# Kernel tuning notes

Measured on AMD Instinct MI355X. Metric: run time of the kernel, lower is better.

The kernel has to match this reference:

```python
import jax, jax.numpy as jnp
import numpy as np

B, L, H, F, D = 8, 2048, 1024, 256, 3  # batch, seq, d_model, adapter bottleneck, non-news domains
EPS = 1e-6  # annotated-transformer LayerNorm eps


def setup_inputs() -> dict:
    key = jax.random.key(0)
    ks = jax.random.split(key, 6)
    s1 = 1.0 / np.sqrt(H)
    s2 = 1.0 / np.sqrt(F)
    return {
        "x": jax.random.normal(ks[0], (B, L, H), jnp.float32),
        # per-domain LayerNorm params (SublayerConnection.norm)
        "ln_g": jnp.ones((D, H), jnp.float32),
        "ln_b": jnp.zeros((D, H), jnp.float32),
        # per-domain adapter FFN: Linear(H->F), ReLU, Linear(F->H)
        "W1": (jax.random.normal(ks[1], (D, F, H), jnp.float32) * s1),
        "b1": jnp.zeros((D, F), jnp.float32),
        "W2": (jax.random.normal(ks[2], (D, H, F), jnp.float32) * s2),
        "b2": jnp.zeros((D, H), jnp.float32),
        # per-domain gate Linear(2H -> 1), split into the x-half (gu) and adapter-half (gv)
        "gu": (jax.random.normal(ks[3], (D, H), jnp.float32) * s1),
        "gv": (jax.random.normal(ks[4], (D, H), jnp.float32) * s1),
        "gb": jnp.zeros((D,), jnp.float32),
    }


def reference(x, ln_g, ln_b, W1, b1, W2, b2, gu, gv, gb):
    # mix_output=True, used_domain_list=['news','book','bible','iwslt'],
    # target_domain='book' (in list -> no extra pass), dropout=eval (identity).
    mu = jnp.mean(x, axis=-1, keepdims=True)
    sd = jnp.std(x, axis=-1, keepdims=True, ddof=1)  # torch .std default (unbiased)
    xn = (x - mu) / (sd + EPS)                        # shared normalization stats
    # per-domain LayerNorm affine -> [D,B,L,H]
    h = xn[None] * ln_g[:, None, None, :] + ln_b[:, None, None, :]
    # adapter FFN (wo_residual_forward): Linear -> ReLU -> Linear
    mid = jax.nn.relu(jnp.einsum('dblh,dfh->dblf', h, W1) + b1[:, None, None, :])
    a = jnp.einsum('dblf,dhf->dblh', mid, W2) + b2[:, None, None, :]  # [D,B,L,H]
    # gate = sigmoid(Linear([x; a])) with W_gate split as [gu | gv]
    gate = jax.nn.sigmoid(
        jnp.einsum('blh,dh->dbl', x, gu)
        + jnp.einsum('dblh,dh->dbl', a, gv)
        + gb[:, None, None]
    )  # [D,B,L]
    # stacked sum includes 'news' contribution (= x), then outer residual +x:
    return 2.0 * x + jnp.sum(gate[..., None] * a, axis=0)
```

## Files before the change

### kernel.cpp

```cpp
#include <hip/hip_runtime.h>
#include <cstdint>

#define T_TOK 16384
#define H 1024
#define F 256
#define D 3
#define DF 768

typedef unsigned short u16;
typedef __attribute__((ext_vector_type(8))) short short8;
typedef __attribute__((ext_vector_type(4))) float floatx4;

__device__ __forceinline__ u16 f2bf(float f) {
  unsigned u = __float_as_uint(f);
  u += 0x7fff + ((u >> 16) & 1);
  return (u16)(u >> 16);
}
__device__ __forceinline__ float bf2f(u16 s) {
  return __uint_as_float(((unsigned)s) << 16);
}

__device__ __forceinline__ void gload_lds16(const void* g, void* l) {
  __builtin_amdgcn_global_load_lds(
      reinterpret_cast<const __attribute__((address_space(1))) void*>(
          reinterpret_cast<uintptr_t>(g)),
      reinterpret_cast<__attribute__((address_space(3))) void*>(
          reinterpret_cast<uintptr_t>(l)),
      16, 0, 0);
}

#define FENCE() asm volatile("" ::: "memory")
#define BAR1() do { FENCE(); __builtin_amdgcn_s_barrier(); \
    asm volatile("s_waitcnt lgkmcnt(0)" ::: "memory"); \
    __builtin_amdgcn_sched_barrier(0); } while (0)
#define BAR2() do { FENCE(); __builtin_amdgcn_s_barrier(); FENCE(); } while (0)
#define VMC(n) asm volatile("s_waitcnt vmcnt(" #n ")" ::: "memory")

__device__ __forceinline__ float block_reduce_256(float v, float* red, int tid) {
  #pragma unroll
  for (int o = 32; o > 0; o >>= 1) v += __shfl_xor(v, o);
  __syncthreads();
  if ((tid & 63) == 0) red[tid >> 6] = v;
  __syncthreads();
  return red[0] + red[1] + red[2] + red[3];
}


__global__ __launch_bounds__(256)
void prep_elem(const float* __restrict__ W1, const float* __restrict__ lng,
               u16* __restrict__ W1p, const float* __restrict__ W2,
               u16* __restrict__ W2r)
{
  int idx = blockIdx.x * 256 + threadIdx.x;
  int stride = gridDim.x * 256;
  for (int i = idx; i < D * F * H; i += stride) {
    int h = i & (H - 1);
    int d = i / (F * H);
    W1p[i] = f2bf(W1[i] * lng[d * H + h]);
  }
  for (int i = idx; i < H * DF; i += stride) {
    int k = i % DF;
    int hh = i / DF;
    int d = k >> 8;
    int f = k & (F - 1);
    W2r[i] = f2bf(W2[((size_t)d * H + hh) * F + f]);
  }
}

__global__ __launch_bounds__(256)
void prep_dots(const float* __restrict__ W1, const float* __restrict__ lnb,
               const float* __restrict__ b1, const float* __restrict__ W2,
               const float* __restrict__ gv, const float* __restrict__ b2,
               const float* __restrict__ gb, float* __restrict__ b1p,
               float* __restrict__ wg, float* __restrict__ cg)
{
  __shared__ float red[4];
  int d = blockIdx.x >> 8;
  int f = blockIdx.x & 255;
  int tid = threadIdx.x;
  float s1 = 0.f, s2 = 0.f, s3 = 0.f;
  for (int h = tid; h < H; h += 256) {
    float w1v = W1[((size_t)d * F + f) * H + h];
    float gvv = gv[d * H + h];
    s1 += lnb[d * H + h] * w1v;
    s2 += W2[((size_t)d * H + h) * F + f] * gvv;
    if (f == 0) s3 += b2[d * H + h] * gvv;
  }
  float S1 = block_reduce_256(s1, red, tid);
  float S2 = block_reduce_256(s2, red, tid);
  if (tid == 0) {
    b1p[d * F + f] = b1[d * F + f] + S1;
    wg[d * F + f] = S2;
  }
  if (f == 0) {
    float S3 = block_reduce_256(s3, red, tid);
    if (tid == 0) cg[d] = gb[d] + S3;
  }
}

__global__ __launch_bounds__(256)
void ln_xu_kernel(const float* __restrict__ x, const float* __restrict__ gu,
                  u16* __restrict__ xn, float* __restrict__ xu)
{
  int t = blockIdx.x;
  int tid = threadIdx.x;
  const float4 xv = *reinterpret_cast<const float4*>(x + (size_t)t * H + tid * 4);
  const float4 g0 = *reinterpret_cast<const float4*>(gu + tid * 4);
  const float4 g1 = *reinterpret_cast<const float4*>(gu + H + tid * 4);
  const float4 g2 = *reinterpret_cast<const float4*>(gu + 2 * H + tid * 4);
  float s  = xv.x + xv.y + xv.z + xv.w;
  float sq = xv.x * xv.x + xv.y * xv.y + xv.z * xv.z + xv.w * xv.w;
  float d0 = xv.x * g0.x + xv.y * g0.y + xv.z * g0.z + xv.w * g0.w;
  float d1 = xv.x * g1.x + xv.y * g1.y + xv.z * g1.z + xv.w * g1.w;
  float d2 = xv.x * g2.x + xv.y * g2.y + xv.z * g2.z + xv.w * g2.w;
  #pragma unroll
  for (int o = 32; o > 0; o >>= 1) {
    s  += __shfl_xor(s, o);  sq += __shfl_xor(sq, o);
    d0 += __shfl_xor(d0, o); d1 += __shfl_xor(d1, o); d2 += __shfl_xor(d2, o);
  }
  __shared__ float red[4][5];
  int w = tid >> 6;
  if ((tid & 63) == 0) {
    red[w][0] = s; red[w][1] = sq; red[w][2] = d0; red[w][3] = d1; red[w][4] = d2;
  }
  __syncthreads();
  float S  = red[0][0] + red[1][0] + red[2][0] + red[3][0];
  float SQ = red[0][1] + red[1][1] + red[2][1] + red[3][1];
  float mu = S * (1.0f / H);
  float var = (SQ - (float)H * mu * mu) * (1.0f / (H - 1));
  float rs = 1.0f / (sqrtf(fmaxf(var, 0.0f)) + 1e-6f);
  ushort4 o4;
  o4.x = f2bf((xv.x - mu) * rs);
  o4.y = f2bf((xv.y - mu) * rs);
  o4.z = f2bf((xv.z - mu) * rs);
  o4.w = f2bf((xv.w - mu) * rs);
  *reinterpret_cast<ushort4*>(xn + (size_t)t * H + tid * 4) = o4;
  if (tid == 0) {
    xu[t]             = red[0][2] + red[1][2] + red[2][2] + red[3][2];
    xu[T_TOK + t]     = red[0][3] + red[1][3] + red[2][3] + red[3][3];
    xu[2 * T_TOK + t] = red[0][4] + red[1][4] + red[2][4] + red[3][4];
  }
}

template <int K, int NLD, int EPI>
__global__ __launch_bounds__(512, 2)
void gemm8(const u16* __restrict__ A, const u16* __restrict__ Bm,
           const float* __restrict__ p0,
           const float* __restrict__ p1,
           const float* __restrict__ p2,
           const float* __restrict__ p3,
           u16* __restrict__ o16,
           float* __restrict__ o32,
           int nBy)
{
  constexpr int NKT = K / 64;
  constexpr int NITER = NKT / 2;
  extern __shared__ u16 LD[];

  const int tid = threadIdx.x, lane = tid & 63, w = tid >> 6;
  const int wm = w >> 2, wn = w & 3, lr = lane & 15, sl = lane >> 4;

  const int nwg = gridDim.x;
  const int wgs = (blockIdx.x & 7) * (nwg >> 3) + (blockIdx.x >> 3);
  const int bx = wgs / nBy, by = wgs % nBy;
  const int m0 = by * 256, n0 = bx * 256;

  const u16* Asrc = A + (size_t)m0 * K;
  const u16* Bsrc = Bm + (size_t)n0 * K;

  const int srow = tid >> 2, ss = tid & 3;
  const int slog = ss ^ ((srow >> 1) & 3);
  const int soff0 = srow * K + slog * 8;
  const int soff1 = (128 + srow) * K + slog * 8;
  const int ldst0 = w * 512;
  const int ldst1 = 4096 + w * 512;

  const int xr = (lr >> 1) & 3;
  const int aoff = (wm * 128 + lr) * 32 + ((sl ^ xr) << 3);
  const int boff = (wn * 64 + lr) * 32 + ((sl ^ xr) << 3);

  floatx4 acc[8][4] = {};
  short8 a[8], b[2];

#define SLOTA(d, kh) (LD + ((d)*4 + (kh)) * 8192)
#define SLOTB(d, kh) (LD + ((d)*4 + 2 + (kh)) * 8192)
#define STG(slot, src, T_, KH) do { \
    int t_ = (T_) < (NKT - 1) ? (T_) : (NKT - 1); \
    int kb_ = t_ * 64 + (KH) * 32; \
    gload_lds16((src) + soff0 + kb_, (slot) + ldst0); \
    gload_lds16((src) + soff1 + kb_, (slot) + ldst1); \
  } while (0)
#define LDA(d, kh) do { const u16* s_ = SLOTA(d, kh) + aoff; \
    _Pragma("unroll") for (int mf_ = 0; mf_ < 8; ++mf_) \
      a[mf_] = *reinterpret_cast<const short8*>(s_ + mf_ * 512); } while (0)
#define LDB(d, kh, nh) do { const u16* s_ = SLOTB(d, kh) + boff + (nh) * 1024; \
    b[0] = *reinterpret_cast<const short8*>(s_); \
    b[1] = *reinterpret_cast<const short8*>(s_ + 512); } while (0)
#define MM(nh) do { __builtin_amdgcn_s_setprio(1); \
    _Pragma("unroll") for (int mf_ = 0; mf_ < 8; ++mf_) { \
      acc[mf_][(nh)*2+0] = __builtin_amdgcn_mfma_f32_16x16x32_bf16(a[mf_], b[0], acc[mf_][(nh)*2+0], 0, 0, 0); \
      acc[mf_][(nh)*2+1] = __builtin_amdgcn_mfma_f32_16x16x32_bf16(a[mf_], b[1], acc[mf_][(nh)*2+1], 0, 0, 0); } \
    __builtin_amdgcn_s_setprio(0); } while (0)

  STG(SLOTA(0, 0), Asrc, 0, 0);
  STG(SLOTB(0, 0), Bsrc, 0, 0);
  STG(SLOTA(0, 1), Asrc, 0, 1);
  STG(SLOTB(0, 1), Bsrc, 0, 1);
  STG(SLOTA(1, 0), Asrc, 1, 0);
  STG(SLOTB(1, 0), Bsrc, 1, 0);
  STG(SLOTA(1, 1), Asrc, 1, 1);
  VMC(10);
  BAR2();

  #pragma unroll 1
  for (int i = 0; i < NITER; ++i) {
    const int kt = 2 * i;
    LDA(0, 0); LDB(0, 0, 0);
    STG(SLOTB(1, 1), Bsrc, kt + 1, 1);
    BAR1(); MM(0); BAR2();
    LDB(0, 0, 1);
    STG(SLOTA(0, 0), Asrc, kt + 2, 0);
    BAR1(); MM(1); VMC(10); BAR2();
    LDA(0, 1); LDB(0, 1, 0);
    STG(SLOTB(0, 0), Bsrc, kt + 2, 0);
    BAR1(); MM(0); BAR2();
    LDB(0, 1, 1);
    STG(SLOTA(0, 1), Asrc, kt + 2, 1);
    BAR1(); MM(1); VMC(10); BAR2();
    LDA(1, 0); LDB(1, 0, 0);
    STG(SLOTB(0, 1), Bsrc, kt + 2, 1);
    BAR1(); MM(0); BAR2();
    LDB(1, 0, 1);
    STG(SLOTA(1, 0), Asrc, kt + 3, 0);
    BAR1(); MM(1); VMC(10); BAR2();
    LDA(1, 1); LDB(1, 1, 0);
    STG(SLOTB(1, 0), Bsrc, kt + 3, 0);
    BAR1(); MM(0); BAR2();
    LDB(1, 1, 1);
    STG(SLOTA(1, 1), Asrc, kt + 3, 1);
    BAR1(); MM(1); VMC(10); BAR2();
  }
  VMC(0);
  BAR2();

  if constexpr (EPI == 1) {
    float b1v[4], wgv[4];
    #pragma unroll
    for (int nf = 0; nf < 4; ++nf) {
      int col = n0 + wn * 64 + nf * 16 + lr;
      b1v[nf] = p0[col];
      wgv[nf] = p1[col];
    }
    float* red = (float*)LD;
    #pragma unroll
    for (int mf = 0; mf < 8; ++mf)
      #pragma unroll
      for (int i2 = 0; i2 < 4; ++i2) {
        float p = 0.f;
        #pragma unroll
        for (int nf = 0; nf < 4; ++nf)
          p += fmaxf(acc[mf][nf][i2] + b1v[nf], 0.f) * wgv[nf];
        p += __shfl_xor(p, 1); p += __shfl_xor(p, 2);
        p += __shfl_xor(p, 4); p += __shfl_xor(p, 8);
        if (lr == 0) red[wn * 256 + wm * 128 + mf * 16 + sl * 4 + i2] = p;
      }
    __syncthreads();
    const int d = bx;
    const float cgv = p3[d];
    #pragma unroll
    for (int mf = 0; mf < 8; ++mf)
      #pragma unroll
      for (int i2 = 0; i2 < 4; ++i2) {
        int rl = wm * 128 + mf * 16 + sl * 4 + i2;
        int r = m0 + rl;
        float logit = red[rl] + red[256 + rl] + red[512 + rl] + red[768 + rl]
                    + p2[(size_t)d * T_TOK + r] + cgv;
        float g = 1.f / (1.f + expf(-logit));
        #pragma unroll
        for (int nf = 0; nf < 4; ++nf) {
          int col = n0 + wn * 64 + nf * 16 + lr;
          float v = fmaxf(acc[mf][nf][i2] + b1v[nf], 0.f);
          o16[(size_t)r * NLD + col] = f2bf(v * g);
        }
        if (lr == 0 && wn == 0) o32[(size_t)d * T_TOK + r] = g;
      }
  } else {
    float b2v[3][4];
    #pragma unroll
    for (int dd = 0; dd < 3; ++dd)
      #pragma unroll
      for (int nf = 0; nf < 4; ++nf)
        b2v[dd][nf] = p2[dd * H + n0 + wn * 64 + nf * 16 + lr];
    #pragma unroll
    for (int mf = 0; mf < 8; ++mf)
      #pragma unroll
      for (int i2 = 0; i2 < 4; ++i2) {
        int r = m0 + wm * 128 + mf * 16 + sl * 4 + i2;
        float g0 = p1[r], g1 = p1[T_TOK + r], g2 = p1[2 * T_TOK + r];
        const float* xrow = p0 + (size_t)r * H;
        float* orow = o32 + (size_t)r * NLD;
        #pragma unroll
        for (int nf = 0; nf < 4; ++nf) {
          int col = n0 + wn * 64 + nf * 16 + lr;
          orow[col] = acc[mf][nf][i2] + 2.f * xrow[col]
                    + g0 * b2v[0][nf] + g1 * b2v[1][nf] + g2 * b2v[2][nf];
        }
      }
  }
#undef SLOTA
#undef SLOTB
#undef STG
#undef LDA
#undef LDB
#undef MM
}


extern "C" void kernel_launch(void* const* d_in, const int* in_sizes, int n_in,
                              void* d_out, int out_size, void* d_ws, size_t ws_size,
                              hipStream_t stream) {
  const float* x   = (const float*)d_in[0];
  const float* lng = (const float*)d_in[1];
  const float* lnb = (const float*)d_in[2];
  const float* W1  = (const float*)d_in[3];
  const float* b1  = (const float*)d_in[4];
  const float* W2  = (const float*)d_in[5];
  const float* b2  = (const float*)d_in[6];
  const float* gu  = (const float*)d_in[7];
  const float* gv  = (const float*)d_in[8];
  const float* gb  = (const float*)d_in[9];
  float* out = (float*)d_out;

  char* ws = (char*)d_ws;
  u16* xn   = (u16*)ws;  ws += (size_t)T_TOK * H * 2;
  u16* mid  = (u16*)ws;  ws += (size_t)T_TOK * DF * 2;
  u16* W1p  = (u16*)ws;  ws += (size_t)DF * H * 2;
  u16* W2r  = (u16*)ws;  ws += (size_t)H * DF * 2;
  float* b1p  = (float*)ws;  ws += DF * 4;
  float* wg   = (float*)ws;  ws += DF * 4;
  float* cg   = (float*)ws;  ws += 256;
  float* xu   = (float*)ws;  ws += (size_t)D * T_TOK * 4;
  float* gate = (float*)ws;  ws += (size_t)D * T_TOK * 4;
  (void)ws_size; (void)in_sizes; (void)n_in; (void)out_size;

  hipFuncSetAttribute(reinterpret_cast<const void*>(&gemm8<1024, DF, 1>),
                      hipFuncAttributeMaxDynamicSharedMemorySize, 131072);
  hipFuncSetAttribute(reinterpret_cast<const void*>(&gemm8<768, H, 2>),
                      hipFuncAttributeMaxDynamicSharedMemorySize, 131072);

  prep_elem<<<3072, 256, 0, stream>>>(W1, lng, W1p, W2, W2r);
  prep_dots<<<DF, 256, 0, stream>>>(W1, lnb, b1, W2, gv, b2, gb, b1p, wg, cg);
  ln_xu_kernel<<<T_TOK, 256, 0, stream>>>(x, gu, xn, xu);
  gemm8<1024, DF, 1><<<64 * 3, 512, 131072, stream>>>(
      xn, W1p, b1p, wg, xu, cg, mid, gate, 64);
  gemm8<768, H, 2><<<64 * 4, 512, 131072, stream>>>(
      mid, W2r, x, gate, b2, nullptr, nullptr, out, 64);
}
```

Baseline: 132.3 us.

## Split MFMA tile by M-halves and peel final K iteration in GEMM pipeline

Reorders the per-wave MFMA sub-tiling so each phase loads 4 A fragments and 4 B fragments (splitting by M halves instead of N halves), changing the LDS read pattern and register footprint. It also reschedules the global-to-LDS staging order and peels the last loop iteration into an epilogue, so no clamped redundant loads are issued past the end of K. This removes wasted tail loads and rebalances LDS reads across phases, at the cost of more code and different wait counts that must line up exactly.

```diff
diff --git a/kernel.cpp b/kernel.cpp
--- a/kernel.cpp
+++ b/kernel.cpp
@@ -180,26 +180,26 @@
   const int boff = (wn * 64 + lr) * 32 + ((sl ^ xr) << 3);
 
   floatx4 acc[8][4] = {};
-  short8 a[8], b[2];
+  short8 a[4], b[4];
 
 #define SLOTA(d, kh) (LD + ((d)*4 + (kh)) * 8192)
 #define SLOTB(d, kh) (LD + ((d)*4 + 2 + (kh)) * 8192)
 #define STG(slot, src, T_, KH) do { \
-    int t_ = (T_) < (NKT - 1) ? (T_) : (NKT - 1); \
-    int kb_ = t_ * 64 + (KH) * 32; \
+    int kb_ = (T_) * 64 + (KH) * 32; \
     gload_lds16((src) + soff0 + kb_, (slot) + ldst0); \
     gload_lds16((src) + soff1 + kb_, (slot) + ldst1); \
   } while (0)
-#define LDA(d, kh) do { const u16* s_ = SLOTA(d, kh) + aoff; \
-    _Pragma("unroll") for (int mf_ = 0; mf_ < 8; ++mf_) \
+#define LDA(d, kh, mh) do { const u16* s_ = SLOTA(d, kh) + aoff + (mh) * 2048; \
+    _Pragma("unroll") for (int mf_ = 0; mf_ < 4; ++mf_) \
       a[mf_] = *reinterpret_cast<const short8*>(s_ + mf_ * 512); } while (0)
-#define LDB(d, kh, nh) do { const u16* s_ = SLOTB(d, kh) + boff + (nh) * 1024; \
-    b[0] = *reinterpret_cast<const short8*>(s_); \
-    b[1] = *reinterpret_cast<const short8*>(s_ + 512); } while (0)
-#define MM(nh) do { __builtin_amdgcn_s_setprio(1); \
-    _Pragma("unroll") for (int mf_ = 0; mf_ < 8; ++mf_) { \
-      acc[mf_][(nh)*2+0] = __builtin_amdgcn_mfma_f32_16x16x32_bf16(a[mf_], b[0], acc[mf_][(nh)*2+0], 0, 0, 0); \
-      acc[mf_][(nh)*2+1] = __builtin_amdgcn_mfma_f32_16x16x32_bf16(a[mf_], b[1], acc[mf_][(nh)*2+1], 0, 0, 0); } \
+#define LDB(d, kh) do { const u16* s_ = SLOTB(d, kh) + boff; \
+    _Pragma("unroll") for (int nf_ = 0; nf_ < 4; ++nf_) \
+      b[nf_] = *reinterpret_cast<const short8*>(s_ + nf_ * 512); } while (0)
+#define MM(mh) do { __builtin_amdgcn_s_setprio(1); \
+    _Pragma("unroll") for (int mf_ = 0; mf_ < 4; ++mf_) \
+      _Pragma("unroll") for (int nf_ = 0; nf_ < 4; ++nf_) \
+        acc[(mh)*4+mf_][nf_] = __builtin_amdgcn_mfma_f32_16x16x32_bf16( \
+            a[mf_], b[nf_], acc[(mh)*4+mf_][nf_], 0, 0, 0); \
     __builtin_amdgcn_s_setprio(0); } while (0)
 
   STG(SLOTA(0, 0), Asrc, 0, 0);
@@ -208,39 +208,58 @@
   STG(SLOTB(0, 1), Bsrc, 0, 1);
   STG(SLOTA(1, 0), Asrc, 1, 0);
   STG(SLOTB(1, 0), Bsrc, 1, 0);
-  STG(SLOTA(1, 1), Asrc, 1, 1);
-  VMC(10);
+  VMC(8);
   BAR2();
 
   #pragma unroll 1
-  for (int i = 0; i < NITER; ++i) {
+  for (int i = 0; i < NITER - 1; ++i) {
     const int kt = 2 * i;
-    LDA(0, 0); LDB(0, 0, 0);
+    LDA(0, 0, 0); LDB(0, 0);
+    STG(SLOTA(1, 1), Asrc, kt + 1, 1);
+    BAR1(); MM(0); BAR2();
+    LDA(0, 0, 1);
     STG(SLOTB(1, 1), Bsrc, kt + 1, 1);
-    BAR1(); MM(0); BAR2();
-    LDB(0, 0, 1);
+    BAR1(); MM(1); VMC(6); BAR2();
+    LDA(0, 1, 0); LDB(0, 1);
     STG(SLOTA(0, 0), Asrc, kt + 2, 0);
-    BAR1(); MM(1); VMC(10); BAR2();
-    LDA(0, 1); LDB(0, 1, 0);
+    BAR1(); MM(0); BAR2();
+    LDA(0, 1, 1);
     STG(SLOTB(0, 0), Bsrc, kt + 2, 0);
-    BAR1(); MM(0); BAR2();
-    LDB(0, 1, 1);
+    BAR1(); MM(1); VMC(6); BAR2();
+    LDA(1, 0, 0); LDB(1, 0);
     STG(SLOTA(0, 1), Asrc, kt + 2, 1);
-    BAR1(); MM(1); VMC(10); BAR2();
-    LDA(1, 0); LDB(1, 0, 0);
+    BAR1(); MM(0); BAR2();
+    LDA(1, 0, 1);
     STG(SLOTB(0, 1), Bsrc, kt + 2, 1);
-    BAR1(); MM(0); BAR2();
-    LDB(1, 0, 1);
+    BAR1(); MM(1); VMC(6); BAR2();
+    LDA(1, 1, 0); LDB(1, 1);
     STG(SLOTA(1, 0), Asrc, kt + 3, 0);
-    BAR1(); MM(1); VMC(10); BAR2();
-    LDA(1, 1); LDB(1, 1, 0);
+    BAR1(); MM(0); BAR2();
+    LDA(1, 1, 1);
     STG(SLOTB(1, 0), Bsrc, kt + 3, 0);
-    BAR1(); MM(0); BAR2();
-    LDB(1, 1, 1);
-    STG(SLOTA(1, 1), Asrc, kt + 3, 1);
-    BAR1(); MM(1); VMC(10); BAR2();
-  }
-  VMC(0);
+    BAR1(); MM(1); VMC(6); BAR2();
+  }
+  {
+    const int kt = NKT - 2;
+    LDA(0, 0, 0); LDB(0, 0);
+    STG(SLOTA(1, 1), Asrc, kt + 1, 1);
+    BAR1(); MM(0); BAR2();
+    LDA(0, 0, 1);
+    STG(SLOTB(1, 1), Bsrc, kt + 1, 1);
+    BAR1(); MM(1); VMC(6); BAR2();
+    LDA(0, 1, 0); LDB(0, 1);
+    BAR1(); MM(0); BAR2();
+    LDA(0, 1, 1);
+    BAR1(); MM(1); VMC(4); BAR2();
+    LDA(1, 0, 0); LDB(1, 0);
+    BAR1(); MM(0); BAR2();
+    LDA(1, 0, 1);
+    BAR1(); MM(1); VMC(0); BAR2();
+    LDA(1, 1, 0); LDB(1, 1);
+    BAR1(); MM(0); BAR2();
+    LDA(1, 1, 1);
+    BAR1(); MM(1); BAR2();
+  }
   BAR2();
 
   if constexpr (EPI == 1) {
```

Measured after the change: 132.9 us. About the same (+0.4%).

## Replace 256x256 double-buffered GEMM with 128x256 tile three-stage pipeline

Applied to the files above, without the earlier changes.

Both GEMMs move from a 256x256 tile with a four-slot, half-K staged schedule to 128x256 tiles using a three-slot ring of 32-wide K steps. The smaller LDS footprint and accumulator set allow higher occupancy (launch bounds 4) and double the workgroup count, which improves load balance on 256 CUs. The tile-to-block mapping now iterates N-fastest so blocks sharing an A row-tile are adjacent. The cost is more global and LDS traffic per FLOP, and the LDS XOR swizzle is dropped, which may add bank conflicts.

```diff
diff --git a/kernel.cpp b/kernel.cpp
--- a/kernel.cpp
+++ b/kernel.cpp
@@ -143,18 +143,18 @@
 }
 
 template <int K, int NLD, int EPI>
-__global__ __launch_bounds__(512, 2)
-void gemm8(const u16* __restrict__ A, const u16* __restrict__ Bm,
-           const float* __restrict__ p0,
-           const float* __restrict__ p1,
-           const float* __restrict__ p2,
-           const float* __restrict__ p3,
-           u16* __restrict__ o16,
-           float* __restrict__ o32,
-           int nBy)
+__global__ __launch_bounds__(512, 4)
+void gemm3s(const u16* __restrict__ A, const u16* __restrict__ Bm,
+            const float* __restrict__ p0,
+            const float* __restrict__ p1,
+            const float* __restrict__ p2,
+            const float* __restrict__ p3,
+            u16* __restrict__ o16,
+            float* __restrict__ o32,
+            int nBx)
 {
-  constexpr int NKT = K / 64;
-  constexpr int NITER = NKT / 2;
+  constexpr int NS = K / 32;
+  constexpr int SLOT = 12288;
   extern __shared__ u16 LD[];
 
   const int tid = threadIdx.x, lane = tid & 63, w = tid >> 6;
@@ -162,85 +162,73 @@
 
   const int nwg = gridDim.x;
   const int wgs = (blockIdx.x & 7) * (nwg >> 3) + (blockIdx.x >> 3);
-  const int bx = wgs / nBy, by = wgs % nBy;
-  const int m0 = by * 256, n0 = bx * 256;
+  const int bx = wgs % nBx, by = wgs / nBx;
+  const int m0 = by * 128, n0 = bx * 256;
 
   const u16* Asrc = A + (size_t)m0 * K;
   const u16* Bsrc = Bm + (size_t)n0 * K;
 
-  const int srow = tid >> 2, ss = tid & 3;
-  const int slog = ss ^ ((srow >> 1) & 3);
-  const int soff0 = srow * K + slog * 8;
-  const int soff1 = (128 + srow) * K + slog * 8;
-  const int ldst0 = w * 512;
-  const int ldst1 = 4096 + w * 512;
-
-  const int xr = (lr >> 1) & 3;
-  const int aoff = (wm * 128 + lr) * 32 + ((sl ^ xr) << 3);
-  const int boff = (wn * 64 + lr) * 32 + ((sl ^ xr) << 3);
-
-  floatx4 acc[8][4] = {};
-  short8 a[8], b[2];
-
-#define SLOTA(d, kh) (LD + ((d)*4 + (kh)) * 8192)
-#define SLOTB(d, kh) (LD + ((d)*4 + 2 + (kh)) * 8192)
-#define STG(slot, src, T_, KH) do { \
-    int t_ = (T_) < (NKT - 1) ? (T_) : (NKT - 1); \
-    int kb_ = t_ * 64 + (KH) * 32; \
-    gload_lds16((src) + soff0 + kb_, (slot) + ldst0); \
-    gload_lds16((src) + soff1 + kb_, (slot) + ldst1); \
+  const int goff0 = (tid >> 2) * K + (tid & 3) * 8;
+  const int goff1 = goff0 + 128 * K;
+  const int w512 = w * 512;
+
+  const int sl8 = sl * 8;
+  const int aoff = (wm * 64 + lr) * 32 + sl8;
+  const int boff = 4096 + (wn * 64 + lr) * 32 + sl8;
+
+  floatx4 acc[4][4] = {};
+  short8 a[4], b[4];
+
+#define STG(P, ks) do { \
+    gload_lds16(Asrc + goff0 + (ks) * 32, (P) + w512); \
+    gload_lds16(Bsrc + goff0 + (ks) * 32, (P) + 4096 + w512); \
+    gload_lds16(Bsrc + goff1 + (ks) * 32, (P) + 8192 + w512); \
   } while (0)
-#define LDA(d, kh) do { const u16* s_ = SLOTA(d, kh) + aoff; \
-    _Pragma("unroll") for (int mf_ = 0; mf_ < 8; ++mf_) \
-      a[mf_] = *reinterpret_cast<const short8*>(s_ + mf_ * 512); } while (0)
-#define LDB(d, kh, nh) do { const u16* s_ = SLOTB(d, kh) + boff + (nh) * 1024; \
-    b[0] = *reinterpret_cast<const short8*>(s_); \
-    b[1] = *reinterpret_cast<const short8*>(s_ + 512); } while (0)
-#define MM(nh) do { __builtin_amdgcn_s_setprio(1); \
-    _Pragma("unroll") for (int mf_ = 0; mf_ < 8; ++mf_) { \
-      acc[mf_][(nh)*2+0] = __builtin_amdgcn_mfma_f32_16x16x32_bf16(a[mf_], b[0], acc[mf_][(nh)*2+0], 0, 0, 0); \
-      acc[mf_][(nh)*2+1] = __builtin_amdgcn_mfma_f32_16x16x32_bf16(a[mf_], b[1], acc[mf_][(nh)*2+1], 0, 0, 0); } \
+#define LDAB(P) do { const u16* sa_ = (P) + aoff; const u16* sb_ = (P) + boff; \
+    _Pragma("unroll") for (int i_ = 0; i_ < 4; ++i_) { \
+      a[i_] = *reinterpret_cast<const short8*>(sa_ + i_ * 512); \
+      b[i_] = *reinterpret_cast<const short8*>(sb_ + i_ * 512); } } while (0)
+#define MM() do { __builtin_amdgcn_s_setprio(1); \
+    _Pragma("unroll") for (int mf_ = 0; mf_ < 4; ++mf_) \
+      _Pragma("unroll") for (int nf_ = 0; nf_ < 4; ++nf_) \
+        acc[mf_][nf_] = __builtin_amdgcn_mfma_f32_16x16x32_bf16( \
+            a[mf_], b[nf_], acc[mf_][nf_], 0, 0, 0); \
     __builtin_amdgcn_s_setprio(0); } while (0)
 
-  STG(SLOTA(0, 0), Asrc, 0, 0);
-  STG(SLOTB(0, 0), Bsrc, 0, 0);
-  STG(SLOTA(0, 1), Asrc, 0, 1);
-  STG(SLOTB(0, 1), Bsrc, 0, 1);
-  STG(SLOTA(1, 0), Asrc, 1, 0);
-  STG(SLOTB(1, 0), Bsrc, 1, 0);
-  STG(SLOTA(1, 1), Asrc, 1, 1);
-  VMC(10);
+  STG(LD, 0);
+  STG(LD + SLOT, 1);
+  VMC(3);
   BAR2();
 
-  #pragma unroll 1
-  for (int i = 0; i < NITER; ++i) {
-    const int kt = 2 * i;
-    LDA(0, 0); LDB(0, 0, 0);
-    STG(SLOTB(1, 1), Bsrc, kt + 1, 1);
-    BAR1(); MM(0); BAR2();
-    LDB(0, 0, 1);
-    STG(SLOTA(0, 0), Asrc, kt + 2, 0);
-    BAR1(); MM(1); VMC(10); BAR2();
-    LDA(0, 1); LDB(0, 1, 0);
-    STG(SLOTB(0, 0), Bsrc, kt + 2, 0);
-    BAR1(); MM(0); BAR2();
-    LDB(0, 1, 1);
-    STG(SLOTA(0, 1), Asrc, kt + 2, 1);
-    BAR1(); MM(1); VMC(10); BAR2();
-    LDA(1, 0); LDB(1, 0, 0);
-    STG(SLOTB(0, 1), Bsrc, kt + 2, 1);
-    BAR1(); MM(0); BAR2();
-    LDB(1, 0, 1);
-    STG(SLOTA(1, 0), Asrc, kt + 3, 0);
-    BAR1(); MM(1); VMC(10); BAR2();
-    LDA(1, 1); LDB(1, 1, 0);
-    STG(SLOTB(1, 0), Bsrc, kt + 3, 0);
-    BAR1(); MM(0); BAR2();
-    LDB(1, 1, 1);
-    STG(SLOTA(1, 1), Asrc, kt + 3, 1);
-    BAR1(); MM(1); VMC(10); BAR2();
-  }
-  VMC(0);
+  int s = 0;
+  #pragma unroll 3
+  for (int p = 0; p < NS - 3; ++p) {
+    u16* cur = LD + s * SLOT;
+    int s2 = s + 2; if (s2 >= 3) s2 -= 3;
+    LDAB(cur);
+    STG(LD + s2 * SLOT, p + 2);
+    BAR1(); MM(); VMC(3); BAR2();
+    ++s; if (s == 3) s = 0;
+  }
+  {
+    u16* cur = LD + s * SLOT;
+    int s2 = s + 2; if (s2 >= 3) s2 -= 3;
+    LDAB(cur);
+    STG(LD + s2 * SLOT, NS - 1);
+    BAR1(); MM(); VMC(3); BAR2();
+    ++s; if (s == 3) s = 0;
+  }
+  {
+    u16* cur = LD + s * SLOT;
+    LDAB(cur);
+    BAR1(); MM(); VMC(0); BAR2();
+    ++s; if (s == 3) s = 0;
+  }
+  {
+    u16* cur = LD + s * SLOT;
+    LDAB(cur);
+    BAR1(); MM(); BAR2();
+  }
   BAR2();
 
   if constexpr (EPI == 1) {
@@ -253,7 +241,7 @@
     }
     float* red = (float*)LD;
     #pragma unroll
-    for (int mf = 0; mf < 8; ++mf)
+    for (int mf = 0; mf < 4; ++mf)
       #pragma unroll
       for (int i2 = 0; i2 < 4; ++i2) {
         float p = 0.f;
@@ -262,18 +250,18 @@
           p += fmaxf(acc[mf][nf][i2] + b1v[nf], 0.f) * wgv[nf];
         p += __shfl_xor(p, 1); p += __shfl_xor(p, 2);
         p += __shfl_xor(p, 4); p += __shfl_xor(p, 8);
-        if (lr == 0) red[wn * 256 + wm * 128 + mf * 16 + sl * 4 + i2] = p;
+        if (lr == 0) red[wn * 128 + wm * 64 + mf * 16 + sl * 4 + i2] = p;
       }
     __syncthreads();
     const int d = bx;
     const float cgv = p3[d];
     #pragma unroll
-    for (int mf = 0; mf < 8; ++mf)
+    for (int mf = 0; mf < 4; ++mf)
       #pragma unroll
       for (int i2 = 0; i2 < 4; ++i2) {
-        int rl = wm * 128 + mf * 16 + sl * 4 + i2;
+        int rl = wm * 64 + mf * 16 + sl * 4 + i2;
         int r = m0 + rl;
-        float logit = red[rl] + red[256 + rl] + red[512 + rl] + red[768 + rl]
+        float logit = red[rl] + red[128 + rl] + red[256 + rl] + red[384 + rl]
                     + p2[(size_t)d * T_TOK + r] + cgv;
         float g = 1.f / (1.f + expf(-logit));
         #pragma unroll
@@ -292,10 +280,10 @@
       for (int nf = 0; nf < 4; ++nf)
         b2v[dd][nf] = p2[dd * H + n0 + wn * 64 + nf * 16 + lr];
     #pragma unroll
-    for (int mf = 0; mf < 8; ++mf)
+    for (int mf = 0; mf < 4; ++mf)
       #pragma unroll
       for (int i2 = 0; i2 < 4; ++i2) {
-        int r = m0 + wm * 128 + mf * 16 + sl * 4 + i2;
+        int r = m0 + wm * 64 + mf * 16 + sl * 4 + i2;
         float g0 = p1[r], g1 = p1[T_TOK + r], g2 = p1[2 * T_TOK + r];
         const float* xrow = p0 + (size_t)r * H;
         float* orow = o32 + (size_t)r * NLD;
@@ -307,11 +295,8 @@
         }
       }
   }
-#undef SLOTA
-#undef SLOTB
 #undef STG
-#undef LDA
-#undef LDB
+#undef LDAB
 #undef MM
 }
 
@@ -343,16 +328,16 @@
   float* gate = (float*)ws;  ws += (size_t)D * T_TOK * 4;
   (void)ws_size; (void)in_sizes; (void)n_in; (void)out_size;
 
-  hipFuncSetAttribute(reinterpret_cast<const void*>(&gemm8<1024, DF, 1>),
-                      hipFuncAttributeMaxDynamicSharedMemorySize, 131072);
-  hipFuncSetAttribute(reinterpret_cast<const void*>(&gemm8<768, H, 2>),
-                      hipFuncAttributeMaxDynamicSharedMemorySize, 131072);
+  hipFuncSetAttribute(reinterpret_cast<const void*>(&gemm3s<1024, DF, 1>),
+                      hipFuncAttributeMaxDynamicSharedMemorySize, 73728);
+  hipFuncSetAttribute(reinterpret_cast<const void*>(&gemm3s<768, H, 2>),
+                      hipFuncAttributeMaxDynamicSharedMemorySize, 73728);
 
   prep_elem<<<3072, 256, 0, stream>>>(W1, lng, W1p, W2, W2r);
   prep_dots<<<DF, 256, 0, stream>>>(W1, lnb, b1, W2, gv, b2, gb, b1p, wg, cg);
   ln_xu_kernel<<<T_TOK, 256, 0, stream>>>(x, gu, xn, xu);
-  gemm8<1024, DF, 1><<<64 * 3, 512, 131072, stream>>>(
-      xn, W1p, b1p, wg, xu, cg, mid, gate, 64);
-  gemm8<768, H, 2><<<64 * 4, 512, 131072, stream>>>(
-      mid, W2r, x, gate, b2, nullptr, nullptr, out, 64);
-}
+  gemm3s<1024, DF, 1><<<128 * 3, 512, 73728, stream>>>(
+      xn, W1p, b1p, wg, xu, cg, mid, gate, 3);
+  gemm3s<768, H, 2><<<128 * 4, 512, 73728, stream>>>(
+      mid, W2r, x, gate, b2, nullptr, nullptr, out, 4);
+}
```

Measured after the change: 131.2 us. Within noise of the previous version (-0.8%).
